# Kernel tuning notes

Measured on AMD Instinct MI355X. Metric: run time of the kernel, lower is better.

The kernel has to match this reference:

```python
import jax, jax.numpy as jnp
import numpy as np

N_NODES = 100000
N_EDGES = 3200000
N_GRAPHS = 64
EPS = 1e-5

def setup_inputs() -> dict:
    key = jax.random.key(0)
    ks = jax.random.split(key, 12)
    x = jax.random.normal(ks[0], (N_NODES, 3), dtype=jnp.float32)
    edge_index = jax.random.randint(ks[1], (2, N_EDGES), 0, N_NODES, dtype=jnp.int64)
    edge_attr = jax.random.uniform(ks[2], (N_EDGES, 2), dtype=jnp.float32)
    batch = jnp.sort(jax.random.randint(ks[3], (N_NODES,), 0, N_GRAPHS, dtype=jnp.int64))
    # SplineConv kernels: [kernel_size^dim = 4, in, out]
    W1 = jax.random.normal(ks[4], (4, 3, 16), dtype=jnp.float32) * 0.3
    g1 = jnp.ones((16,), jnp.float32); b1 = jnp.zeros((16,), jnp.float32)
    W2 = jax.random.normal(ks[5], (4, 16, 32), dtype=jnp.float32) * 0.15
    g2 = jnp.ones((32,), jnp.float32); b2 = jnp.zeros((32,), jnp.float32)
    fc_w = jax.random.normal(ks[6], (10, 32), dtype=jnp.float32) * 0.15
    return {"x": x, "edge_index": edge_index, "edge_attr": edge_attr, "batch": batch,
            "W1": W1, "g1": g1, "b1": b1, "W2": W2, "g2": g2, "b2": b2, "fc_w": fc_w}

def _spline_basis(edge_attr):
    # degree=1, kernel_size=2, open spline: v = p*(K-degree)=p in [0,1), floor(v)=0
    # per-dim weights (1-p, p); flattened kernel index k = i0 + 2*i1
    p0, p1 = edge_attr[:, 0], edge_attr[:, 1]
    w0 = jnp.stack([1.0 - p0, p0], axis=-1)  # [E,2] over i0
    w1 = jnp.stack([1.0 - p1, p1], axis=-1)  # [E,2] over i1
    return (w1[:, :, None] * w0[:, None, :]).reshape(-1, 4)  # [E,4], k=i0+2*i1

def _spline_conv(x, src, dst, basis, W, n_nodes):
    # message per edge: sum_k basis[e,k] * (x[src[e]] @ W[k]); mean-aggregate at dst
    msg = jnp.einsum('ek,kio,ei->eo', basis, W, x[src])
    agg = jax.ops.segment_sum(msg, dst, num_segments=n_nodes)
    cnt = jax.ops.segment_sum(jnp.ones((src.shape[0],), x.dtype), dst, num_segments=n_nodes)
    return agg / jnp.maximum(cnt, 1.0)[:, None]

def _batchnorm(x, gamma, beta):
    mu = jnp.mean(x, axis=0)
    var = jnp.mean((x - mu) ** 2, axis=0)  # biased, as torch uses for normalization
    return (x - mu) * jax.lax.rsqrt(var + EPS) * gamma + beta

def reference(x, edge_index, edge_attr, batch, W1, g1, b1, W2, g2, b2, fc_w):
    src, dst = edge_index[0], edge_index[1]
    basis = _spline_basis(edge_attr)  # [E,4]
    h = jax.nn.elu(_spline_conv(x, src, dst, basis, W1, N_NODES))
    h = _batchnorm(h, g1, b1)
    h = jax.nn.elu(_spline_conv(h, src, dst, basis, W2, N_NODES))
    h = _batchnorm(h, g2, b2)
    # global mean pool over graphs
    s = jax.ops.segment_sum(h, batch, num_segments=N_GRAPHS)
    c = jax.ops.segment_sum(jnp.ones((h.shape[0],), h.dtype), batch, num_segments=N_GRAPHS)
    gm = s / jnp.maximum(c, 1.0)[:, None]
    return gm @ fc_w.T  # [N_GRAPHS, 10]
```

## Files before the change

kernel.cpp:

```cpp
#include <hip/hip_runtime.h>
#include <math.h>

#define NN 100000
#define NE 3200000
#define NG 64
#define EPSF 1e-5f
#define NB 391
#define BSH 8

#define OFF_ST1     0
#define OFF_ST2     32
#define OFF_GPOOL   96
#define OFF_BCNT    2144
#define ZERO_FLOATS 2536
#define OFF_BBASE   2536
#define OFF_BCUR    2928
#define OFF_OFFS    3320
#define OFF_STARTS  103324
#define OFF_H1      103392
#define OFF_H2      1703392
#define OFF_RECSA   4903392
#define OFF_RECSB   11303392

__device__ __forceinline__ void atomAdd(float* p, float v) {
#if defined(__gfx90a__) || defined(__gfx940__) || defined(__gfx941__) || defined(__gfx942__) || defined(__gfx950__)
    unsafeAtomicAdd(p, v);
#else
    atomicAdd(p, v);
#endif
}

__device__ __forceinline__ float eluf(float x) { return x > 0.f ? x : expm1f(x); }

#define INV32767 (1.f / 32767.f)

__global__ void starts_k(const int* __restrict__ batch, int* __restrict__ starts) {
    int g = threadIdx.x;
    if (g > NG) return;
    int lo = 0, hi = NN;
    while (lo < hi) { int mid = (lo + hi) >> 1; if (batch[mid] < g) lo = mid + 1; else hi = mid; }
    starts[g] = lo;
}

__global__ void __launch_bounds__(256) bcount_k(const int* __restrict__ ei,
                                                int* __restrict__ bcnt) {
    __shared__ int lh[NB];
    int tid = threadIdx.x;
    for (int i = tid; i < NB; i += 256) lh[i] = 0;
    __syncthreads();
    const int4* d4 = (const int4*)(ei + NE);
    int base4 = blockIdx.x * 2048;
#pragma unroll
    for (int j = 0; j < 8; ++j) {
        int idx = base4 + j * 256 + tid;
        if (idx < NE / 4) {
            int4 d = d4[idx];
            atomicAdd(&lh[d.x >> BSH], 1);
            atomicAdd(&lh[d.y >> BSH], 1);
            atomicAdd(&lh[d.z >> BSH], 1);
            atomicAdd(&lh[d.w >> BSH], 1);
        }
    }
    __syncthreads();
    for (int i = tid; i < NB; i += 256)
        if (lh[i] > 0) atomicAdd(&bcnt[i], lh[i]);
}

__global__ void bscan_k(const int* __restrict__ bcnt, int* __restrict__ bbase,
                        int* __restrict__ bcur, int* __restrict__ offs) {
    __shared__ int s[512];
    int tid = threadIdx.x;
    int v = (tid < NB) ? bcnt[tid] : 0;
    s[tid] = v;
    __syncthreads();
    for (int d = 1; d < 512; d <<= 1) {
        int t = (tid >= (unsigned)d) ? s[tid - d] : 0;
        __syncthreads();
        s[tid] += t;
        __syncthreads();
    }
    if (tid < NB) {
        int e = s[tid] - v;
        bbase[tid] = e;
        bcur[tid] = e;
    }
    if (tid == 0) { bbase[NB] = NE; offs[NN] = NE; }
}

__global__ void __launch_bounds__(256) passA(const int* __restrict__ ei,
        const float* __restrict__ ea, int* __restrict__ bcur,
        uint2* __restrict__ recsA) {
    __shared__ int lh[NB];
    __shared__ int gcur[NB];
    int tid = threadIdx.x;
    for (int i = tid; i < NB; i += 256) lh[i] = 0;
    __syncthreads();
    int base = blockIdx.x * 4096;
    uint2 rec[16];
    int bk[16];
#pragma unroll
    for (int j = 0; j < 16; ++j) {
        int e = base + j * 256 + tid;
        bk[j] = -1;
        if (e < NE) {
            int src = ei[e];
            int dst = ei[NE + e];
            float2 p = ((const float2*)ea)[e];
            unsigned q0 = (unsigned)__float2uint_rn(p.x * 32767.f);
            unsigned q1 = (unsigned)__float2uint_rn(p.y * 32767.f);
            rec[j] = make_uint2((unsigned)src | (q0 << 17), (unsigned)dst | (q1 << 17));
            bk[j] = dst >> BSH;
            atomicAdd(&lh[bk[j]], 1);
        }
    }
    __syncthreads();
    for (int i = tid; i < NB; i += 256)
        if (lh[i] > 0) gcur[i] = atomicAdd(&bcur[i], lh[i]);
    __syncthreads();
#pragma unroll
    for (int j = 0; j < 16; ++j) {
        if (bk[j] >= 0) {
            int pos = atomicAdd(&gcur[bk[j]], 1);
            recsA[pos] = rec[j];
        }
    }
}

__global__ void __launch_bounds__(256) fine_k(const int* __restrict__ bbase,
        const uint2* __restrict__ recsA, int* __restrict__ offs,
        uint2* __restrict__ recsB) {
    __shared__ int cnt[256];
    __shared__ int sc[256];
    __shared__ int cur[256];
    int b = blockIdx.x;
    int tid = threadIdx.x;
    int rbeg = bbase[b], rend = bbase[b + 1];
    cnt[tid] = 0;
    __syncthreads();
    for (int i = rbeg + tid; i < rend; i += 256) {
        int d = (int)(recsA[i].y & 0x1FFFFu) & 255;
        atomicAdd(&cnt[d], 1);
    }
    __syncthreads();
    int v = cnt[tid];
    sc[tid] = v;
    __syncthreads();
    for (int d = 1; d < 256; d <<= 1) {
        int t = (tid >= (unsigned)d) ? sc[tid - d] : 0;
        __syncthreads();
        sc[tid] += t;
        __syncthreads();
    }
    int excl = sc[tid] - v;
    cur[tid] = excl;
    int node = (b << BSH) + tid;
    if (node < NN) offs[node] = rbeg + excl;
    __syncthreads();
    for (int i = rbeg + tid; i < rend; i += 256) {
        uint2 rc = recsA[i];
        int d = (int)(rc.y & 0x1FFFFu) & 255;
        int rank = atomicAdd(&cur[d], 1);
        recsB[rbeg + rank] = rc;
    }
}

__global__ void __launch_bounds__(256) conv1_gather(const int* __restrict__ offs,
        const uint2* __restrict__ recs, const float* __restrict__ x,
        const float* __restrict__ W1, float* __restrict__ h1) {
    __shared__ float sW[192];
    if (threadIdx.x < 192) sW[threadIdx.x] = W1[threadIdx.x];
    __syncthreads();
    int n = blockIdx.x * blockDim.x + threadIdx.x;
    if (n >= NN) return;
    int off = offs[n], end = offs[n + 1];
    float T[12];
#pragma unroll
    for (int i = 0; i < 12; ++i) T[i] = 0.f;
    for (int e = off; e < end; ++e) {
        uint2 r = recs[e];
        int s = (int)(r.x & 0x1FFFFu);
        float p0 = (float)(r.x >> 17) * INV32767;
        float p1 = (float)(r.y >> 17) * INV32767;
        float b0 = (1.f - p1) * (1.f - p0), b1 = (1.f - p1) * p0;
        float b2 = p1 * (1.f - p0), b3 = p1 * p0;
        float x0 = x[3 * s], x1 = x[3 * s + 1], x2 = x[3 * s + 2];
        T[0] = fmaf(b0, x0, T[0]);  T[1] = fmaf(b0, x1, T[1]);  T[2]  = fmaf(b0, x2, T[2]);
        T[3] = fmaf(b1, x0, T[3]);  T[4] = fmaf(b1, x1, T[4]);  T[5]  = fmaf(b1, x2, T[5]);
        T[6] = fmaf(b2, x0, T[6]);  T[7] = fmaf(b2, x1, T[7]);  T[8]  = fmaf(b2, x2, T[8]);
        T[9] = fmaf(b3, x0, T[9]);  T[10]= fmaf(b3, x1, T[10]); T[11] = fmaf(b3, x2, T[11]);
    }
    float inv = 1.f / fmaxf((float)(end - off), 1.f);
    float ov[16];
#pragma unroll
    for (int o = 0; o < 16; ++o) {
        float acc = 0.f;
#pragma unroll
        for (int k = 0; k < 4; ++k)
#pragma unroll
            for (int i = 0; i < 3; ++i)
                acc = fmaf(T[k * 3 + i], sW[k * 48 + i * 16 + o], acc);
        acc *= inv;
        ov[o] = eluf(acc);
    }
    float4* hp = (float4*)(h1 + (long)n * 16);
#pragma unroll
    for (int q = 0; q < 4; ++q)
        hp[q] = make_float4(ov[4 * q], ov[4 * q + 1], ov[4 * q + 2], ov[4 * q + 3]);
}

template <int C>
__global__ void bn_sum(const float* __restrict__ h, float* __restrict__ st) {
    __shared__ float ss[C], sq[C];
    if (threadIdx.x < C) { ss[threadIdx.x] = 0.f; sq[threadIdx.x] = 0.f; }
    __syncthreads();
    const int total = NN * C;
    const int stride = gridDim.x * blockDim.x;
    float a = 0.f, q = 0.f;
    for (int i = blockIdx.x * blockDim.x + threadIdx.x; i < total; i += stride) {
        float v = h[i];
        a += v; q += v * v;
    }
#pragma unroll
    for (int d = C; d < 64; d <<= 1) { a += __shfl_xor(a, d); q += __shfl_xor(q, d); }
    int lane = threadIdx.x & 63;
    if (lane < C) { atomicAdd(&ss[lane], a); atomicAdd(&sq[lane], q); }
    __syncthreads();
    if (threadIdx.x < C) {
        atomAdd(&st[threadIdx.x], ss[threadIdx.x]);
        atomAdd(&st[C + threadIdx.x], sq[threadIdx.x]);
    }
}

__global__ void __launch_bounds__(256) conv2_gather(const int* __restrict__ offs,
        const uint2* __restrict__ recs, const float* __restrict__ h1,
        const float* __restrict__ st1, const float* __restrict__ g1,
        const float* __restrict__ b1v, const float* __restrict__ W2,
        float* __restrict__ h2) {
    __shared__ float s_sc[16], s_sh[16];
    __shared__ float sWp[2048];
    __shared__ float sV[128];
    if (threadIdx.x < 16) {
        int c = threadIdx.x;
        float mu = st1[c] * (1.f / NN);
        float var = st1[16 + c] * (1.f / NN) - mu * mu;
        float rs = rsqrtf(var + EPSF);
        float s = g1[c] * rs;
        s_sc[c] = s;
        s_sh[c] = b1v[c] - mu * s;
    }
    __syncthreads();
    for (int idx = threadIdx.x; idx < 2048; idx += blockDim.x) {
        int i = (idx & 511) >> 5;
        sWp[idx] = s_sc[i] * W2[idx];
    }
    if (threadIdx.x < 128) {
        int k = threadIdx.x >> 5, o = threadIdx.x & 31;
        float acc = 0.f;
#pragma unroll
        for (int i = 0; i < 16; ++i) acc = fmaf(s_sh[i], W2[k * 512 + i * 32 + o], acc);
        sV[threadIdx.x] = acc;
    }
    __syncthreads();
    int n = blockIdx.x * blockDim.x + threadIdx.x;
    if (n >= NN) return;
    int off = offs[n], end = offs[n + 1];
    float U[64];
    float S0 = 0.f, S1 = 0.f, S2 = 0.f, S3 = 0.f;
#pragma unroll
    for (int i = 0; i < 64; ++i) U[i] = 0.f;
    for (int e = off; e < end; ++e) {
        uint2 r = recs[e];
        int s = (int)(r.x & 0x1FFFFu);
        float p0 = (float)(r.x >> 17) * INV32767;
        float p1 = (float)(r.y >> 17) * INV32767;
        float b0 = (1.f - p1) * (1.f - p0), b1 = (1.f - p1) * p0;
        float b2 = p1 * (1.f - p0), b3 = p1 * p0;
        const float4* hp = (const float4*)(h1 + (long)s * 16);
        float4 t0 = hp[0], t1 = hp[1], t2 = hp[2], t3 = hp[3];
        float hv[16] = {t0.x, t0.y, t0.z, t0.w, t1.x, t1.y, t1.z, t1.w,
                        t2.x, t2.y, t2.z, t2.w, t3.x, t3.y, t3.z, t3.w};
#pragma unroll
        for (int i = 0; i < 16; ++i) {
            U[i]      = fmaf(b0, hv[i], U[i]);
            U[16 + i] = fmaf(b1, hv[i], U[16 + i]);
            U[32 + i] = fmaf(b2, hv[i], U[32 + i]);
            U[48 + i] = fmaf(b3, hv[i], U[48 + i]);
        }
        S0 += b0; S1 += b1; S2 += b2; S3 += b3;
    }
    float inv = 1.f / fmaxf((float)(end - off), 1.f);
    float4 acc[8];
#pragma unroll
    for (int ob = 0; ob < 8; ++ob) acc[ob] = make_float4(0.f, 0.f, 0.f, 0.f);
    const float4* Wp4 = (const float4*)sWp;
#pragma unroll 4
    for (int ki = 0; ki < 64; ++ki) {
        float u = U[ki];
#pragma unroll
        for (int ob = 0; ob < 8; ++ob) {
            float4 w = Wp4[ki * 8 + ob];
            acc[ob].x = fmaf(u, w.x, acc[ob].x);
            acc[ob].y = fmaf(u, w.y, acc[ob].y);
            acc[ob].z = fmaf(u, w.z, acc[ob].z);
            acc[ob].w = fmaf(u, w.w, acc[ob].w);
        }
    }
    const float4* V4 = (const float4*)sV;
    float Sarr[4] = {S0, S1, S2, S3};
#pragma unroll
    for (int k = 0; k < 4; ++k) {
        float u = Sarr[k];
#pragma unroll
        for (int ob = 0; ob < 8; ++ob) {
            float4 w = V4[k * 8 + ob];
            acc[ob].x = fmaf(u, w.x, acc[ob].x);
            acc[ob].y = fmaf(u, w.y, acc[ob].y);
            acc[ob].z = fmaf(u, w.z, acc[ob].z);
            acc[ob].w = fmaf(u, w.w, acc[ob].w);
        }
    }
    float4* out4 = (float4*)(h2 + (long)n * 32);
#pragma unroll
    for (int ob = 0; ob < 8; ++ob) {
        float4 a = acc[ob];
        a.x = eluf(a.x * inv); a.y = eluf(a.y * inv);
        a.z = eluf(a.z * inv); a.w = eluf(a.w * inv);
        out4[ob] = a;
    }
}

__global__ void pool_k(const float* __restrict__ h2pre, const float* __restrict__ st2,
                       const float* __restrict__ g2, const float* __restrict__ b2v,
                       const int* __restrict__ batch, float* __restrict__ gpool) {
    int t = blockIdx.x * blockDim.x + threadIdx.x;
    int c = t & 31;
    int chunk = t >> 5;
    if (chunk >= NN / 32) return;
    float mu = st2[c] * (1.f / NN);
    float var = st2[32 + c] * (1.f / NN) - mu * mu;
    float rs = rsqrtf(var + EPSF);
    float s = g2[c] * rs;
    float sh = b2v[c] - mu * s;
    int n0 = chunk * 32;
    int g_cur = batch[n0];
    float acc = 0.f;
    for (int i = 0; i < 32; ++i) {
        int n = n0 + i;
        int g = batch[n];
        float v = fmaf(h2pre[(long)n * 32 + c], s, sh);
        if (g != g_cur) {
            atomAdd(gpool + g_cur * 32 + c, acc);
            acc = 0.f;
            g_cur = g;
        }
        acc += v;
    }
    atomAdd(gpool + g_cur * 32 + c, acc);
}

__global__ void final_k(const float* __restrict__ gpool, const int* __restrict__ starts,
                        const float* __restrict__ fc, float* __restrict__ out) {
    int t = blockIdx.x * blockDim.x + threadIdx.x;
    if (t >= NG * 10) return;
    int g = t / 10, j = t - g * 10;
    float cg = (float)(starts[g + 1] - starts[g]);
    float inv = 1.f / fmaxf(cg, 1.f);
    float sv = 0.f;
#pragma unroll
    for (int ch = 0; ch < 32; ++ch) sv = fmaf(gpool[g * 32 + ch], fc[j * 32 + ch], sv);
    out[t] = sv * inv;
}

extern "C" void kernel_launch(void* const* d_in, const int* in_sizes, int n_in,
                              void* d_out, int out_size, void* d_ws, size_t ws_size,
                              hipStream_t stream) {
    const float* x     = (const float*)d_in[0];
    const int*   ei    = (const int*)d_in[1];
    const float* ea    = (const float*)d_in[2];
    const int*   batch = (const int*)d_in[3];
    const float* W1    = (const float*)d_in[4];
    const float* g1    = (const float*)d_in[5];
    const float* b1v   = (const float*)d_in[6];
    const float* W2    = (const float*)d_in[7];
    const float* g2    = (const float*)d_in[8];
    const float* b2v   = (const float*)d_in[9];
    const float* fc    = (const float*)d_in[10];
    float* ws = (float*)d_ws;

    float*  st1    = ws + OFF_ST1;
    float*  st2    = ws + OFF_ST2;
    float*  gpool  = ws + OFF_GPOOL;
    int*    bcnt   = (int*)(ws + OFF_BCNT);
    int*    bbase  = (int*)(ws + OFF_BBASE);
    int*    bcur   = (int*)(ws + OFF_BCUR);
    int*    offs   = (int*)(ws + OFF_OFFS);
    int*    starts = (int*)(ws + OFF_STARTS);
    float*  h1     = ws + OFF_H1;
    float*  h2     = ws + OFF_H2;
    uint2*  recsA  = (uint2*)(ws + OFF_RECSA);
    uint2*  recsB  = (uint2*)(ws + OFF_RECSB);

    hipMemsetAsync(ws, 0, (size_t)ZERO_FLOATS * sizeof(float), stream);
    starts_k<<<1, 128, 0, stream>>>(batch, starts);

    const int BLK = 256;
    const int NGRID = (NN + BLK - 1) / BLK;

    bcount_k<<<391, BLK, 0, stream>>>(ei, bcnt);
    bscan_k<<<1, 512, 0, stream>>>(bcnt, bbase, bcur, offs);
    passA<<<(NE + 4095) / 4096, BLK, 0, stream>>>(ei, ea, bcur, recsA);
    fine_k<<<NB, BLK, 0, stream>>>(bbase, recsA, offs, recsB);
    conv1_gather<<<NGRID, BLK, 0, stream>>>(offs, recsB, x, W1, h1);
    bn_sum<16><<<512, BLK, 0, stream>>>(h1, st1);
    conv2_gather<<<NGRID, BLK, 0, stream>>>(offs, recsB, h1, st1, g1, b1v, W2, h2);
    bn_sum<32><<<512, BLK, 0, stream>>>(h2, st2);
    pool_k<<<NGRID, BLK, 0, stream>>>(h2, st2, g2, b2v, batch, gpool);
    final_k<<<3, BLK, 0, stream>>>(gpool, starts, fc, (float*)d_out);
}
```

Measured before the change: 381.3 us.

## Split each node's edge gather across four lanes and store h1 in fp16

Both conv gather kernels now assign four threads to each destination node. Each thread strides over that node's edge list, and the partial results are combined with warp shuffles, which gives more parallelism and better latency hiding for high-degree nodes. The intermediate h1 is stored as half precision, which halves its write traffic and the random-gather traffic in conv2; the BN-stat kernel is adapted to read half2. The costs are fp16 rounding error in h1, redundant projection work in three of the four lanes, and heavy register pressure in conv2 from 64 accumulators plus the shuffles.

```diff
diff --git a/kernel.cpp b/kernel.cpp
--- a/kernel.cpp
+++ b/kernel.cpp
@@ -1,4 +1,5 @@
 #include <hip/hip_runtime.h>
+#include <hip/hip_fp16.h>
 #include <math.h>
 
 #define NN 100000
@@ -18,9 +19,9 @@
 #define OFF_OFFS    3320
 #define OFF_STARTS  103324
 #define OFF_H1      103392
-#define OFF_H2      1703392
-#define OFF_RECSA   4903392
-#define OFF_RECSB   11303392
+#define OFF_H2      903392
+#define OFF_RECSA   4103392
+#define OFF_RECSB   10503392
 
 __device__ __forceinline__ void atomAdd(float* p, float v) {
 #if defined(__gfx90a__) || defined(__gfx940__) || defined(__gfx941__) || defined(__gfx942__) || defined(__gfx950__)
@@ -166,17 +167,18 @@
 
 __global__ void __launch_bounds__(256) conv1_gather(const int* __restrict__ offs,
         const uint2* __restrict__ recs, const float* __restrict__ x,
-        const float* __restrict__ W1, float* __restrict__ h1) {
+        const float* __restrict__ W1, __half* __restrict__ h1) {
     __shared__ float sW[192];
     if (threadIdx.x < 192) sW[threadIdx.x] = W1[threadIdx.x];
     __syncthreads();
-    int n = blockIdx.x * blockDim.x + threadIdx.x;
+    int t = blockIdx.x * blockDim.x + threadIdx.x;
+    int n = t >> 2, sub = t & 3;
     if (n >= NN) return;
     int off = offs[n], end = offs[n + 1];
     float T[12];
 #pragma unroll
     for (int i = 0; i < 12; ++i) T[i] = 0.f;
-    for (int e = off; e < end; ++e) {
+    for (int e = off + sub; e < end; e += 4) {
         uint2 r = recs[e];
         int s = (int)(r.x & 0x1FFFFu);
         float p0 = (float)(r.x >> 17) * INV32767;
@@ -189,7 +191,6 @@
         T[6] = fmaf(b2, x0, T[6]);  T[7] = fmaf(b2, x1, T[7]);  T[8]  = fmaf(b2, x2, T[8]);
         T[9] = fmaf(b3, x0, T[9]);  T[10]= fmaf(b3, x1, T[10]); T[11] = fmaf(b3, x2, T[11]);
     }
-    float inv = 1.f / fmaxf((float)(end - off), 1.f);
     float ov[16];
 #pragma unroll
     for (int o = 0; o < 16; ++o) {
@@ -199,40 +200,75 @@
 #pragma unroll
             for (int i = 0; i < 3; ++i)
                 acc = fmaf(T[k * 3 + i], sW[k * 48 + i * 16 + o], acc);
-        acc *= inv;
-        ov[o] = eluf(acc);
-    }
-    float4* hp = (float4*)(h1 + (long)n * 16);
-#pragma unroll
-    for (int q = 0; q < 4; ++q)
-        hp[q] = make_float4(ov[4 * q], ov[4 * q + 1], ov[4 * q + 2], ov[4 * q + 3]);
-}
-
-template <int C>
-__global__ void bn_sum(const float* __restrict__ h, float* __restrict__ st) {
-    __shared__ float ss[C], sq[C];
-    if (threadIdx.x < C) { ss[threadIdx.x] = 0.f; sq[threadIdx.x] = 0.f; }
-    __syncthreads();
-    const int total = NN * C;
+        acc += __shfl_xor(acc, 1);
+        acc += __shfl_xor(acc, 2);
+        ov[o] = acc;
+    }
+    if (sub != 0) return;
+    float inv = 1.f / fmaxf((float)(end - off), 1.f);
+    __half2 hh[8];
+#pragma unroll
+    for (int q = 0; q < 8; ++q)
+        hh[q] = __float22half2_rn(make_float2(eluf(ov[2 * q] * inv),
+                                              eluf(ov[2 * q + 1] * inv)));
+    uint4* hp = (uint4*)(h1 + (long)n * 16);
+    hp[0] = *(uint4*)&hh[0];
+    hp[1] = *(uint4*)&hh[4];
+}
+
+__global__ void bn_sum16h(const __half2* __restrict__ h, float* __restrict__ st) {
+    __shared__ float ss[16], sq[16];
+    if (threadIdx.x < 16) { ss[threadIdx.x] = 0.f; sq[threadIdx.x] = 0.f; }
+    __syncthreads();
+    const int total = NN * 8;
+    const int stride = gridDim.x * blockDim.x;
+    float a0 = 0.f, a1 = 0.f, q0 = 0.f, q1 = 0.f;
+    for (int i = blockIdx.x * blockDim.x + threadIdx.x; i < total; i += stride) {
+        float2 f = __half22float2(h[i]);
+        a0 += f.x; q0 += f.x * f.x;
+        a1 += f.y; q1 += f.y * f.y;
+    }
+#pragma unroll
+    for (int d = 8; d < 64; d <<= 1) {
+        a0 += __shfl_xor(a0, d); q0 += __shfl_xor(q0, d);
+        a1 += __shfl_xor(a1, d); q1 += __shfl_xor(q1, d);
+    }
+    int lane = threadIdx.x & 63;
+    if (lane < 8) {
+        atomicAdd(&ss[2 * lane], a0);     atomicAdd(&sq[2 * lane], q0);
+        atomicAdd(&ss[2 * lane + 1], a1); atomicAdd(&sq[2 * lane + 1], q1);
+    }
+    __syncthreads();
+    if (threadIdx.x < 16) {
+        atomAdd(&st[threadIdx.x], ss[threadIdx.x]);
+        atomAdd(&st[16 + threadIdx.x], sq[threadIdx.x]);
+    }
+}
+
+__global__ void bn_sum32(const float* __restrict__ h, float* __restrict__ st) {
+    __shared__ float ss[32], sq[32];
+    if (threadIdx.x < 32) { ss[threadIdx.x] = 0.f; sq[threadIdx.x] = 0.f; }
+    __syncthreads();
+    const int total = NN * 32;
     const int stride = gridDim.x * blockDim.x;
     float a = 0.f, q = 0.f;
     for (int i = blockIdx.x * blockDim.x + threadIdx.x; i < total; i += stride) {
         float v = h[i];
         a += v; q += v * v;
     }
-#pragma unroll
-    for (int d = C; d < 64; d <<= 1) { a += __shfl_xor(a, d); q += __shfl_xor(q, d); }
+    a += __shfl_xor(a, 32);
+    q += __shfl_xor(q, 32);
     int lane = threadIdx.x & 63;
-    if (lane < C) { atomicAdd(&ss[lane], a); atomicAdd(&sq[lane], q); }
-    __syncthreads();
-    if (threadIdx.x < C) {
+    if (lane < 32) { atomicAdd(&ss[lane], a); atomicAdd(&sq[lane], q); }
+    __syncthreads();
+    if (threadIdx.x < 32) {
         atomAdd(&st[threadIdx.x], ss[threadIdx.x]);
-        atomAdd(&st[C + threadIdx.x], sq[threadIdx.x]);
+        atomAdd(&st[32 + threadIdx.x], sq[threadIdx.x]);
     }
 }
 
 __global__ void __launch_bounds__(256) conv2_gather(const int* __restrict__ offs,
-        const uint2* __restrict__ recs, const float* __restrict__ h1,
+        const uint2* __restrict__ recs, const __half* __restrict__ h1,
         const float* __restrict__ st1, const float* __restrict__ g1,
         const float* __restrict__ b1v, const float* __restrict__ W2,
         float* __restrict__ h2) {
@@ -261,24 +297,33 @@
         sV[threadIdx.x] = acc;
     }
     __syncthreads();
-    int n = blockIdx.x * blockDim.x + threadIdx.x;
+    int t = blockIdx.x * blockDim.x + threadIdx.x;
+    int n = t >> 2, sub = t & 3;
     if (n >= NN) return;
     int off = offs[n], end = offs[n + 1];
     float U[64];
     float S0 = 0.f, S1 = 0.f, S2 = 0.f, S3 = 0.f;
 #pragma unroll
     for (int i = 0; i < 64; ++i) U[i] = 0.f;
-    for (int e = off; e < end; ++e) {
+    for (int e = off + sub; e < end; e += 4) {
         uint2 r = recs[e];
         int s = (int)(r.x & 0x1FFFFu);
         float p0 = (float)(r.x >> 17) * INV32767;
         float p1 = (float)(r.y >> 17) * INV32767;
         float b0 = (1.f - p1) * (1.f - p0), b1 = (1.f - p1) * p0;
         float b2 = p1 * (1.f - p0), b3 = p1 * p0;
-        const float4* hp = (const float4*)(h1 + (long)s * 16);
-        float4 t0 = hp[0], t1 = hp[1], t2 = hp[2], t3 = hp[3];
-        float hv[16] = {t0.x, t0.y, t0.z, t0.w, t1.x, t1.y, t1.z, t1.w,
-                        t2.x, t2.y, t2.z, t2.w, t3.x, t3.y, t3.z, t3.w};
+        const uint4* hp = (const uint4*)(h1 + (long)s * 16);
+        uint4 ua = hp[0], ub = hp[1];
+        float2 f0 = __half22float2(*(const __half2*)&ua.x);
+        float2 f1 = __half22float2(*(const __half2*)&ua.y);
+        float2 f2 = __half22float2(*(const __half2*)&ua.z);
+        float2 f3 = __half22float2(*(const __half2*)&ua.w);
+        float2 f4 = __half22float2(*(const __half2*)&ub.x);
+        float2 f5 = __half22float2(*(const __half2*)&ub.y);
+        float2 f6 = __half22float2(*(const __half2*)&ub.z);
+        float2 f7 = __half22float2(*(const __half2*)&ub.w);
+        float hv[16] = {f0.x, f0.y, f1.x, f1.y, f2.x, f2.y, f3.x, f3.y,
+                        f4.x, f4.y, f5.x, f5.y, f6.x, f6.y, f7.x, f7.y};
 #pragma unroll
         for (int i = 0; i < 16; ++i) {
             U[i]      = fmaf(b0, hv[i], U[i]);
@@ -288,7 +333,6 @@
         }
         S0 += b0; S1 += b1; S2 += b2; S3 += b3;
     }
-    float inv = 1.f / fmaxf((float)(end - off), 1.f);
     float4 acc[8];
 #pragma unroll
     for (int ob = 0; ob < 8; ++ob) acc[ob] = make_float4(0.f, 0.f, 0.f, 0.f);
@@ -319,6 +363,15 @@
             acc[ob].w = fmaf(u, w.w, acc[ob].w);
         }
     }
+#pragma unroll
+    for (int ob = 0; ob < 8; ++ob) {
+        acc[ob].x += __shfl_xor(acc[ob].x, 1); acc[ob].x += __shfl_xor(acc[ob].x, 2);
+        acc[ob].y += __shfl_xor(acc[ob].y, 1); acc[ob].y += __shfl_xor(acc[ob].y, 2);
+        acc[ob].z += __shfl_xor(acc[ob].z, 1); acc[ob].z += __shfl_xor(acc[ob].z, 2);
+        acc[ob].w += __shfl_xor(acc[ob].w, 1); acc[ob].w += __shfl_xor(acc[ob].w, 2);
+    }
+    if (sub != 0) return;
+    float inv = 1.f / fmaxf((float)(end - off), 1.f);
     float4* out4 = (float4*)(h2 + (long)n * 32);
 #pragma unroll
     for (int ob = 0; ob < 8; ++ob) {
@@ -395,7 +448,7 @@
     int*    bcur   = (int*)(ws + OFF_BCUR);
     int*    offs   = (int*)(ws + OFF_OFFS);
     int*    starts = (int*)(ws + OFF_STARTS);
-    float*  h1     = ws + OFF_H1;
+    __half* h1     = (__half*)(ws + OFF_H1);
     float*  h2     = ws + OFF_H2;
     uint2*  recsA  = (uint2*)(ws + OFF_RECSA);
     uint2*  recsB  = (uint2*)(ws + OFF_RECSB);
@@ -404,16 +457,16 @@
     starts_k<<<1, 128, 0, stream>>>(batch, starts);
 
     const int BLK = 256;
-    const int NGRID = (NN + BLK - 1) / BLK;
+    const int NGRID4 = (NN * 4 + BLK - 1) / BLK;
 
     bcount_k<<<391, BLK, 0, stream>>>(ei, bcnt);
     bscan_k<<<1, 512, 0, stream>>>(bcnt, bbase, bcur, offs);
     passA<<<(NE + 4095) / 4096, BLK, 0, stream>>>(ei, ea, bcur, recsA);
     fine_k<<<NB, BLK, 0, stream>>>(bbase, recsA, offs, recsB);
-    conv1_gather<<<NGRID, BLK, 0, stream>>>(offs, recsB, x, W1, h1);
-    bn_sum<16><<<512, BLK, 0, stream>>>(h1, st1);
-    conv2_gather<<<NGRID, BLK, 0, stream>>>(offs, recsB, h1, st1, g1, b1v, W2, h2);
-    bn_sum<32><<<512, BLK, 0, stream>>>(h2, st2);
-    pool_k<<<NGRID, BLK, 0, stream>>>(h2, st2, g2, b2v, batch, gpool);
+    conv1_gather<<<NGRID4, BLK, 0, stream>>>(offs, recsB, x, W1, h1);
+    bn_sum16h<<<512, BLK, 0, stream>>>((const __half2*)h1, st1);
+    conv2_gather<<<NGRID4, BLK, 0, stream>>>(offs, recsB, h1, st1, g1, b1v, W2, h2);
+    bn_sum32<<<512, BLK, 0, stream>>>(h2, st2);
+    pool_k<<<(NN + BLK - 1) / BLK, BLK, 0, stream>>>(h2, st2, g2, b2v, batch, gpool);
     final_k<<<3, BLK, 0, stream>>>(gpool, starts, fc, (float*)d_out);
 }
```

Result: no change. 376.0 us (-1.4%).
